# Kernel optimization log

Measured on AMD Instinct MI355X. Metric: run time of the kernel, lower is better.

Reference implementation:

```python
import jax, jax.numpy as jnp
import numpy as np

HEADS = 32
MAX_PERIOD = 10000.0
EPS = 1e-5


def layernorm(x, w, b):
    m = x.mean(-1, keepdims=True)
    v = ((x - m) ** 2).mean(-1, keepdims=True)
    return (x - m) * jax.lax.rsqrt(v + EPS) * w + b


def apply_rope(q, k, pos):
    # q, k: [B, T, H, D]; pos: [B, T] integer positions
    D = q.shape[-1]
    ds = D // 2
    inv_freq = 1.0 / (MAX_PERIOD ** (jnp.arange(ds, dtype=jnp.float32) / ds))
    ang = pos[..., None].astype(jnp.float32) * inv_freq          # [B, T, ds]
    cos = jnp.cos(ang)[:, :, None, :]                             # [B, T, 1, ds]
    sin = jnp.sin(ang)[:, :, None, :]

    def rot(t):
        tr, ti = t[..., 0::2], t[..., 1::2]
        out_r = tr * cos - ti * sin
        out_i = tr * sin + ti * cos
        return jnp.stack([out_r, out_i], axis=-1).reshape(t.shape)

    return rot(q), rot(k)


def setup_inputs() -> dict:
    key = jax.random.key(0)
    ks = jax.random.split(key, 8)
    B, T, C, F = 2, 1024, 2048, 8192
    H, D = HEADS, C // HEADS
    cap = 1024
    s = 0.02
    return {
        "x": jax.random.normal(ks[0], (B, T, C), jnp.float32),
        "cache": jnp.zeros((2, B, H, cap, D), jnp.float32),
        "in_proj_w": jax.random.normal(ks[1], (3 * C, C), jnp.float32) * s,
        "out_proj_w": jax.random.normal(ks[2], (C, C), jnp.float32) * s,
        "ln1_w": jnp.ones((C,), jnp.float32),
        "ln1_b": jnp.zeros((C,), jnp.float32),
        "ln2_w": jnp.ones((C,), jnp.float32),
        "ln2_b": jnp.zeros((C,), jnp.float32),
        "lin1_w": jax.random.normal(ks[3], (F, C), jnp.float32) * s,
        "lin2_w": jax.random.normal(ks[4], (C, F), jnp.float32) * s,
        "offset": jnp.zeros((B,), jnp.int64 if jax.config.jax_enable_x64 else jnp.int32),
        "end_offset": jnp.zeros((B,), jnp.int64 if jax.config.jax_enable_x64 else jnp.int32),
        "context": 512,
    }


def reference(x, cache, in_proj_w, out_proj_w, ln1_w, ln1_b, ln2_w, ln2_b,
              lin1_w, lin2_w, offset, end_offset, context):
    B, T, C = x.shape
    H = HEADS
    D = C // H
    cap = cache.shape[3]

    # ---- self-attention block ----
    h = layernorm(x, ln1_w, ln1_b)
    qkv = (h @ in_proj_w.T).reshape(B, T, 3, H, D)
    q, k, v = qkv[:, :, 0], qkv[:, :, 1], qkv[:, :, 2]           # [B, T, H, D]

    pos_q = offset[:, None] + jnp.arange(T)                       # [B, T]
    q, k = apply_rope(q, k, pos_q)

    q = q.transpose(0, 2, 1, 3)                                   # [B, H, T, D]
    k = k.transpose(0, 2, 1, 3)
    v = v.transpose(0, 2, 1, 3)

    # circular KV-cache update (functional version of `complete`)
    idx = (jnp.arange(T) + end_offset[:, None]) % cap             # [B, T]

    def upd(c, t, i):  # c: [H, cap, D], t: [H, T, D], i: [T]
        return c.at[:, i, :].set(t)

    keys = jax.vmap(upd)(cache[0], k, idx)                        # [B, H, cap, D]
    values = jax.vmap(upd)(cache[1], v, idx)

    slots = jnp.arange(cap)
    last = end_offset + T - 1                                     # [B]
    end_index = last % cap
    delta = slots[None, :] - end_index[:, None]                   # [B, cap]
    positions = jnp.where(delta <= 0, last[:, None] + delta,
                          last[:, None] + delta - cap)
    invalid = slots[None, :] >= (end_offset + T)[:, None]
    positions = jnp.where(invalid, -1, positions)                 # [B, cap]

    # sliding-window causal mask
    d = pos_q[:, :, None] - positions[:, None, :]                 # [B, T, cap]
    mask = (positions[:, None, :] >= 0) & (d >= 0) & (d < context)

    scale = 1.0 / jnp.sqrt(jnp.asarray(D, jnp.float32))
    scores = jnp.einsum('bhtd,bhsd->bhts', q, keys) * scale
    scores = jnp.where(mask[:, None], scores, jnp.asarray(-1e30, scores.dtype))
    attn = jax.nn.softmax(scores, axis=-1)
    o = jnp.einsum('bhts,bhsd->bhtd', attn, values)
    o = o.transpose(0, 2, 1, 3).reshape(B, T, C)
    x = x + o @ out_proj_w.T

    # ---- feed-forward block ----
    h2 = layernorm(x, ln2_w, ln2_b)
    ff = jax.nn.gelu(h2 @ lin1_w.T, approximate=False) @ lin2_w.T
    return x + ff
```

## Files before the change

kernel.cpp:

```cpp
#include <hip/hip_runtime.h>

typedef __attribute__((ext_vector_type(8))) short bf16x8;
typedef __attribute__((ext_vector_type(4))) float f32x4;
typedef __attribute__((ext_vector_type(8))) short short8v;
typedef __attribute__((ext_vector_type(4))) float float4v;

#define DEV static __device__ __forceinline__

DEV short f2bf(float f) {
  unsigned u = __builtin_bit_cast(unsigned, f);
  u = (u + 0x7fffu + ((u >> 16) & 1u)) >> 16;
  return (short)u;
}
DEV float bf2f(short s) {
  unsigned u = ((unsigned)(unsigned short)s) << 16;
  return __builtin_bit_cast(float, u);
}

DEV void gload_lds16(const void* g, void* l) {
  __builtin_amdgcn_global_load_lds((const __attribute__((address_space(1))) void*)g,
                                   (__attribute__((address_space(3))) void*)l, 16, 0, 0);
}

__global__ __launch_bounds__(256) void cvt_kernel(const float* __restrict__ src,
                                                  short* __restrict__ dst, int n8) {
  int i = blockIdx.x * 256 + threadIdx.x;
  const int stride = gridDim.x * 256;
  for (; i < n8; i += stride) {
    float4v a = ((const float4v*)src)[i * 2];
    float4v b = ((const float4v*)src)[i * 2 + 1];
    short8v o;
    o[0] = f2bf(a.x); o[1] = f2bf(a.y); o[2] = f2bf(a.z); o[3] = f2bf(a.w);
    o[4] = f2bf(b.x); o[5] = f2bf(b.y); o[6] = f2bf(b.z); o[7] = f2bf(b.w);
    ((short8v*)dst)[i] = o;
  }
}

__global__ __launch_bounds__(256) void ln_kernel(const float* __restrict__ x,
                                                 const float* __restrict__ w,
                                                 const float* __restrict__ b,
                                                 short* __restrict__ out) {
  const int C = 2048;
  const int row = blockIdx.x;
  const int tid = threadIdx.x;
  const float* xr = x + (size_t)row * C;
  float xv[8];
  *(float4v*)(xv) = *(const float4v*)(xr + tid * 8);
  *(float4v*)(xv + 4) = *(const float4v*)(xr + tid * 8 + 4);
  float s = 0.f, ss = 0.f;
#pragma unroll
  for (int i = 0; i < 8; ++i) { s += xv[i]; ss += xv[i] * xv[i]; }
#pragma unroll
  for (int d = 1; d < 64; d <<= 1) { s += __shfl_xor(s, d); ss += __shfl_xor(ss, d); }
  __shared__ float red[8];
  const int lane = tid & 63, wv = tid >> 6;
  if (lane == 0) { red[wv] = s; red[4 + wv] = ss; }
  __syncthreads();
  s = red[0] + red[1] + red[2] + red[3];
  ss = red[4] + red[5] + red[6] + red[7];
  const float mean = s * (1.f / 2048.f);
  const float var = ss * (1.f / 2048.f) - mean * mean;
  const float rs = rsqrtf(var + 1e-5f);
  float wv8[8], bv8[8];
  *(float4v*)(wv8) = *(const float4v*)(w + tid * 8);
  *(float4v*)(wv8 + 4) = *(const float4v*)(w + tid * 8 + 4);
  *(float4v*)(bv8) = *(const float4v*)(b + tid * 8);
  *(float4v*)(bv8 + 4) = *(const float4v*)(b + tid * 8 + 4);
  short8v o;
#pragma unroll
  for (int i = 0; i < 8; ++i) o[i] = f2bf((xv[i] - mean) * rs * wv8[i] + bv8[i]);
  *(short8v*)(out + (size_t)row * C + tid * 8) = o;
}

template <int EPI>
__global__ __launch_bounds__(512, 2) void gemm256(const short* __restrict__ A,
                                                  const short* __restrict__ Bw,
                                                  void* __restrict__ C0, void* __restrict__ C1,
                                                  void* __restrict__ C2, void* __restrict__ C3,
                                                  int N, int K, int kChunk, int kTiles) {
  extern __shared__ short smem[];
  const int tid = threadIdx.x;
  const int lane = tid & 63;
  const int wv = tid >> 6;
  const int wr = wv >> 2;
  const int wc = wv & 3;
  const int m0 = blockIdx.y * 256;
  const int n0 = blockIdx.x * 256;
  const int kBegin = blockIdx.z * kChunk;

  const int l15 = lane & 15;
  const int lg = lane >> 4;

  const int fa0 = tid, fa1 = tid + 512;
  const int rA0 = fa0 >> 2, rA1 = fa1 >> 2;
  const int cA0 = (((fa0 & 3) ^ ((rA0 >> 1) & 3))) * 8;
  const int cA1 = (((fa1 & 3) ^ ((rA1 >> 1) & 3))) * 8;

  const short* Asrc0 = A + (size_t)(m0 + rA0) * K + kBegin + cA0;
  const short* Asrc1 = A + (size_t)(m0 + rA1) * K + kBegin + cA1;
  const short* Bsrc0 = Bw + (size_t)(n0 + rA0) * K + kBegin + cA0;
  const short* Bsrc1 = Bw + (size_t)(n0 + rA1) * K + kBegin + cA1;

  f32x4 acc[8][4] = {};

#define STAGE(t)                                                        \
  {                                                                     \
    short* dstb = smem + (((t) & 3) * 16384);                           \
    const size_t ko = (size_t)(t) * 32;                                 \
    gload_lds16(Asrc0 + ko, dstb + fa0 * 8);                            \
    gload_lds16(Asrc1 + ko, dstb + fa1 * 8);                            \
    gload_lds16(Bsrc0 + ko, dstb + 8192 + fa0 * 8);                     \
    gload_lds16(Bsrc1 + ko, dstb + 8192 + fa1 * 8);                     \
  }

  const int pre = kTiles < 3 ? kTiles : 3;
  for (int p = 0; p < pre; ++p) STAGE(p);

  for (int t = 0; t < kTiles; ++t) {
    const int rem = kTiles - 1 - t;
    if (rem >= 2) {
      asm volatile("s_waitcnt vmcnt(8)" ::: "memory");
    } else if (rem == 1) {
      asm volatile("s_waitcnt vmcnt(4)" ::: "memory");
    } else {
      asm volatile("s_waitcnt vmcnt(0)" ::: "memory");
    }
    __builtin_amdgcn_sched_barrier(0);
    __builtin_amdgcn_s_barrier();
    __builtin_amdgcn_sched_barrier(0);

    if (t + 3 < kTiles) STAGE(t + 3);

    const short* sa = smem + ((t & 3) * 16384);
    const short* sb = sa + 8192;
    bf16x8 af[8], bf[4];
#pragma unroll
    for (int m = 0; m < 8; ++m) {
      const int row = wr * 128 + m * 16 + l15;
      af[m] = *(const bf16x8*)(sa + row * 32 + ((lg ^ ((row >> 1) & 3)) * 8));
    }
#pragma unroll
    for (int n = 0; n < 4; ++n) {
      const int row = wc * 64 + n * 16 + l15;
      bf[n] = *(const bf16x8*)(sb + row * 32 + ((lg ^ ((row >> 1) & 3)) * 8));
    }
    __builtin_amdgcn_s_setprio(1);
#pragma unroll
    for (int m = 0; m < 8; ++m)
#pragma unroll
      for (int n = 0; n < 4; ++n)
        acc[m][n] = __builtin_amdgcn_mfma_f32_16x16x32_bf16(af[m], bf[n], acc[m][n], 0, 0, 0);
    __builtin_amdgcn_s_setprio(0);
  }
#undef STAGE

  void* Cout = blockIdx.z == 0 ? C0 : blockIdx.z == 1 ? C1 : blockIdx.z == 2 ? C2 : C3;
#pragma unroll
  for (int m = 0; m < 8; ++m) {
#pragma unroll
    for (int n = 0; n < 4; ++n) {
#pragma unroll
      for (int r = 0; r < 4; ++r) {
        const size_t idx =
            (size_t)(m0 + wr * 128 + m * 16 + lg * 4 + r) * N + (n0 + wc * 64 + n * 16 + l15);
        const float v = acc[m][n][r];
        if (EPI == 0) {
          ((short*)Cout)[idx] = f2bf(v);
        } else if (EPI == 2) {
          const float gl = 0.5f * v * (1.f + erff(v * 0.70710678118f));
          ((short*)Cout)[idx] = f2bf(gl);
        } else {
          ((float*)Cout)[idx] = v;
        }
      }
    }
  }
}

__global__ __launch_bounds__(256) void reduce_k(float* __restrict__ dst,
                                                const float* __restrict__ resid,
                                                const float* __restrict__ p1,
                                                const float* __restrict__ p2,
                                                const float* __restrict__ p3,
                                                int ns, int n4) {
  int i = blockIdx.x * 256 + threadIdx.x;
  const int stride = gridDim.x * 256;
  for (; i < n4; i += stride) {
    float4v d = ((const float4v*)dst)[i];
    float4v r = ((const float4v*)resid)[i];
    float4v a = ((const float4v*)p1)[i];
    d.x += r.x + a.x; d.y += r.y + a.y; d.z += r.z + a.z; d.w += r.w + a.w;
    if (ns == 4) {
      float4v b = ((const float4v*)p2)[i];
      float4v c = ((const float4v*)p3)[i];
      d.x += b.x + c.x; d.y += b.y + c.y; d.z += b.z + c.z; d.w += b.w + c.w;
    }
    ((float4v*)dst)[i] = d;
  }
}

__global__ __launch_bounds__(256) void rope_kernel(const short* __restrict__ qkv,
                                                   short* __restrict__ qo,
                                                   short* __restrict__ ko,
                                                   short* __restrict__ vo,
                                                   const int* __restrict__ offset) {
  const int T = 1024, H = 32;
  const int g = blockIdx.x * 256 + threadIdx.x;
  const int j = g & 31;
  const int h = (g >> 5) & 31;
  const int t = (g >> 10) & 1023;
  const int b = g >> 20;
  const size_t inb = (size_t)(b * T + t) * 6144 + h * 64 + 2 * j;
  const size_t outb = (size_t)((b * H + h) * T + t) * 64 + 2 * j;
  const int pos = offset[b] + t;
  const float ang = (float)pos * __builtin_exp2f(-13.287712379549449f * (float)j * (1.f / 32.f));
  float sn, c;
  __sincosf(ang, &sn, &c);
  const float qr = bf2f(qkv[inb]), qi = bf2f(qkv[inb + 1]);
  qo[outb] = f2bf(qr * c - qi * sn);
  qo[outb + 1] = f2bf(qr * sn + qi * c);
  const float kr = bf2f(qkv[inb + 2048]), ki = bf2f(qkv[inb + 2048 + 1]);
  ko[outb] = f2bf(kr * c - ki * sn);
  ko[outb + 1] = f2bf(kr * sn + ki * c);
  vo[outb] = qkv[inb + 4096];
  vo[outb + 1] = qkv[inb + 4096 + 1];
}

__global__ __launch_bounds__(256) void attn_kernel(const short* __restrict__ qb,
                                                   const short* __restrict__ kb,
                                                   const short* __restrict__ vb,
                                                   short* __restrict__ o,
                                                   const int* __restrict__ offset,
                                                   const int* __restrict__ end_offset,
                                                   const int* __restrict__ ctxp) {
  const int T = 1024;
  __shared__ short Ks[64 * 64];
  __shared__ short Vt[64 * 64];
  __shared__ short Ps[4][16 * 64];
  const int tid = threadIdx.x;
  const int lane = tid & 63;
  const int w = tid >> 6;
  const int blk = blockIdx.x;
  const int qt = blk & 15;
  const int bh = blk >> 4;
  const int b = bh >> 5;
  const int h = bh & 31;
  const int q0 = qt * 64;
  const int offq = offset[b];
  const int offk = end_offset[b];
  const int W = ctxp[0];
  const int odelta = offq - offk;

  const short* qp = qb + (size_t)bh * T * 64;
  const short* kp = kb + (size_t)bh * T * 64;
  const short* vp = vb + (size_t)bh * T * 64;

  const int l15 = lane & 15;
  const int lg = lane >> 4;

  bf16x8 qf[2];
  {
    const int qrow = q0 + w * 16 + l15;
    qf[0] = *(const bf16x8*)(qp + (size_t)qrow * 64 + lg * 8);
    qf[1] = *(const bf16x8*)(qp + (size_t)qrow * 64 + 32 + lg * 8);
  }

  f32x4 oacc[4] = {};
  float mrow[4] = {-1e30f, -1e30f, -1e30f, -1e30f};
  float ssum[4] = {0.f, 0.f, 0.f, 0.f};

  int kv_lo = q0 + odelta - (W - 1);
  if (kv_lo < 0) kv_lo = 0;
  int kv_hi = q0 + 63 + odelta;
  if (kv_hi > T - 1) kv_hi = T - 1;

  for (int t0 = (kv_lo & ~63); t0 <= kv_hi; t0 += 64) {
    __syncthreads();
#pragma unroll
    for (int j = 0; j < 2; ++j) {
      const int r0 = (j * 4 + w) * 8;
      gload_lds16(kp + (size_t)(t0 + r0 + (lane >> 3)) * 64 + (lane & 7) * 8, Ks + r0 * 64);
    }
#pragma unroll
    for (int j = 0; j < 2; ++j) {
      const int kv = (tid >> 3) + j * 32;
      const int d0 = (tid & 7) * 8;
      bf16x8 vv = *(const bf16x8*)(vp + (size_t)(t0 + kv) * 64 + d0);
#pragma unroll
      for (int i = 0; i < 8; ++i) Vt[(d0 + i) * 64 + kv] = vv[i];
    }
    __syncthreads();

    f32x4 s[4] = {};
#pragma unroll
    for (int n = 0; n < 4; ++n) {
      bf16x8 k0f = *(const bf16x8*)(Ks + (n * 16 + l15) * 64 + lg * 8);
      bf16x8 k1f = *(const bf16x8*)(Ks + (n * 16 + l15) * 64 + 32 + lg * 8);
      s[n] = __builtin_amdgcn_mfma_f32_16x16x32_bf16(qf[0], k0f, s[n], 0, 0, 0);
      s[n] = __builtin_amdgcn_mfma_f32_16x16x32_bf16(qf[1], k1f, s[n], 0, 0, 0);
    }

#pragma unroll
    for (int r = 0; r < 4; ++r) {
      const int tq = q0 + w * 16 + lg * 4 + r;
      float sv[4];
      float mx = -1e30f;
#pragma unroll
      for (int n = 0; n < 4; ++n) {
        const int tk = t0 + n * 16 + l15;
        const int dd = tq + odelta - tk;
        const bool valid = (dd >= 0) && (dd < W);
        sv[n] = valid ? s[n][r] * 0.125f : -1e30f;
        mx = fmaxf(mx, sv[n]);
      }
      mx = fmaxf(mx, __shfl_xor(mx, 1));
      mx = fmaxf(mx, __shfl_xor(mx, 2));
      mx = fmaxf(mx, __shfl_xor(mx, 4));
      mx = fmaxf(mx, __shfl_xor(mx, 8));
      const float mnew = fmaxf(mrow[r], mx);
      const float sf = __expf(mrow[r] - mnew);
      mrow[r] = mnew;
      float ls = 0.f;
#pragma unroll
      for (int n = 0; n < 4; ++n) {
        const float p = (sv[n] > -0.5e30f) ? __expf(sv[n] - mnew) : 0.f;
        ls += p;
        Ps[w][(lg * 4 + r) * 64 + n * 16 + l15] = f2bf(p);
      }
      ls += __shfl_xor(ls, 1);
      ls += __shfl_xor(ls, 2);
      ls += __shfl_xor(ls, 4);
      ls += __shfl_xor(ls, 8);
      ssum[r] = ssum[r] * sf + ls;
#pragma unroll
      for (int n = 0; n < 4; ++n) oacc[n][r] *= sf;
    }

#pragma unroll
    for (int ks = 0; ks < 2; ++ks) {
      bf16x8 pa = *(const bf16x8*)(&Ps[w][l15 * 64 + ks * 32 + lg * 8]);
#pragma unroll
      for (int n = 0; n < 4; ++n) {
        bf16x8 vf = *(const bf16x8*)(Vt + (n * 16 + l15) * 64 + ks * 32 + lg * 8);
        oacc[n] = __builtin_amdgcn_mfma_f32_16x16x32_bf16(pa, vf, oacc[n], 0, 0, 0);
      }
    }
  }

#pragma unroll
  for (int n = 0; n < 4; ++n) {
#pragma unroll
    for (int r = 0; r < 4; ++r) {
      const int tq = q0 + w * 16 + lg * 4 + r;
      const float val = oacc[n][r] / ssum[r];
      o[(size_t)(b * T + tq) * 2048 + h * 64 + n * 16 + l15] = f2bf(val);
    }
  }
}

extern "C" void kernel_launch(void* const* d_in, const int* in_sizes, int n_in,
                              void* d_out, int out_size, void* d_ws, size_t ws_size,
                              hipStream_t stream) {
  (void)in_sizes; (void)n_in; (void)out_size;
  const float* x          = (const float*)d_in[0];
  const float* in_proj_w  = (const float*)d_in[2];
  const float* out_proj_w = (const float*)d_in[3];
  const float* ln1_w      = (const float*)d_in[4];
  const float* ln1_b      = (const float*)d_in[5];
  const float* ln2_w      = (const float*)d_in[6];
  const float* ln2_b      = (const float*)d_in[7];
  const float* lin1_w     = (const float*)d_in[8];
  const float* lin2_w     = (const float*)d_in[9];
  const int* offset       = (const int*)d_in[10];
  const int* end_offset   = (const int*)d_in[11];
  const int* ctx          = (const int*)d_in[12];
  float* out = (float*)d_out;

  hipFuncSetAttribute((const void*)gemm256<0>, hipFuncAttributeMaxDynamicSharedMemorySize, 131072);
  hipFuncSetAttribute((const void*)gemm256<2>, hipFuncAttributeMaxDynamicSharedMemorySize, 131072);
  hipFuncSetAttribute((const void*)gemm256<3>, hipFuncAttributeMaxDynamicSharedMemorySize, 131072);

  const size_t MiB = 1048576;
  char* ws = (char*)d_ws;
  float* x1    = (float*)(ws);
  short* hbuf  = (short*)(ws + 16 * MiB);
  short* qkv   = (short*)(ws + 24 * MiB);
  short* qr    = (short*)(ws + 48 * MiB);
  short* kr    = (short*)(ws + 56 * MiB);
  short* vr    = (short*)(ws + 64 * MiB);
  short* wb_in = (short*)(ws + 48 * MiB);
  short* wb_out= (short*)(ws + 24 * MiB);
  float* p1o   = (float*)(ws + 32 * MiB);
  short* g     = (short*)(ws + 24 * MiB);
  short* wb1   = (short*)(ws + 64 * MiB);
  short* wb2   = (short*)(ws + 56 * MiB);
  float* p1f   = (float*)(ws + 72 * MiB);
  float* p2f   = (float*)(ws + 88 * MiB);
  float* p3f   = (float*)(ws + 104 * MiB);
  const int NS_FF2 = (ws_size >= 121 * MiB) ? 4 : 2;

  ln_kernel<<<2048, 256, 0, stream>>>(x, ln1_w, ln1_b, hbuf);
  cvt_kernel<<<2048, 256, 0, stream>>>(in_proj_w, wb_in, 12582912 / 8);
  gemm256<0><<<dim3(24, 8, 1), 512, 131072, stream>>>(hbuf, wb_in, qkv, nullptr, nullptr, nullptr,
                                                      6144, 2048, 2048, 64);
  rope_kernel<<<8192, 256, 0, stream>>>(qkv, qr, kr, vr, offset);
  attn_kernel<<<1024, 256, 0, stream>>>(qr, kr, vr, hbuf, offset, end_offset, ctx);
  cvt_kernel<<<2048, 256, 0, stream>>>(out_proj_w, wb_out, 4194304 / 8);
  gemm256<3><<<dim3(8, 8, 2), 512, 131072, stream>>>(hbuf, wb_out, x1, p1o, nullptr, nullptr,
                                                     2048, 2048, 1024, 32);
  reduce_k<<<1024, 256, 0, stream>>>(x1, x, p1o, nullptr, nullptr, 2, 1048576);
  ln_kernel<<<2048, 256, 0, stream>>>(x1, ln2_w, ln2_b, hbuf);
  cvt_kernel<<<2048, 256, 0, stream>>>(lin1_w, wb1, 16777216 / 8);
  gemm256<2><<<dim3(32, 8, 1), 512, 131072, stream>>>(hbuf, wb1, g, nullptr, nullptr, nullptr,
                                                      8192, 2048, 2048, 64);
  cvt_kernel<<<2048, 256, 0, stream>>>(lin2_w, wb2, 16777216 / 8);
  if (NS_FF2 == 4) {
    gemm256<3><<<dim3(8, 8, 4), 512, 131072, stream>>>(g, wb2, out, p1f, p2f, p3f,
                                                       2048, 8192, 2048, 64);
    reduce_k<<<1024, 256, 0, stream>>>(out, x1, p1f, p2f, p3f, 4, 1048576);
  } else {
    gemm256<3><<<dim3(8, 8, 2), 512, 131072, stream>>>(g, wb2, out, p1f, nullptr, nullptr,
                                                       2048, 8192, 4096, 128);
    reduce_k<<<1024, 256, 0, stream>>>(out, x1, p1f, nullptr, nullptr, 2, 1048576);
  }
}
```

Before: 432.6 us.

## Remap GEMM tiles per XCD, deepen out-proj split-K, bf16 FF2 partials

Block indices in the GEMM are remapped so each group of 8 consecutive blocks (one per XCD) covers a compact rectangle of output tiles. The aim is better L2 reuse of A and B tiles within each XCD's cache. The out-projection split-K goes from 2 to 4 slices to raise parallelism. The FF2 GEMM is fixed at 2-way split-K with the second partial stored as bf16 and merged by a new reduction kernel, which cuts partial-sum traffic at some precision cost.

```diff
diff --git a/kernel.cpp b/kernel.cpp
--- a/kernel.cpp
+++ b/kernel.cpp
@@ -53,8 +53,8 @@
 #pragma unroll
   for (int d = 1; d < 64; d <<= 1) { s += __shfl_xor(s, d); ss += __shfl_xor(ss, d); }
   __shared__ float red[8];
-  const int lane = tid & 63, wv = tid >> 6;
-  if (lane == 0) { red[wv] = s; red[4 + wv] = ss; }
+  const int lane = tid & 63, wvv = tid >> 6;
+  if (lane == 0) { red[wvv] = s; red[4 + wvv] = ss; }
   __syncthreads();
   s = red[0] + red[1] + red[2] + red[3];
   ss = red[4] + red[5] + red[6] + red[7];
@@ -77,15 +77,19 @@
                                                   const short* __restrict__ Bw,
                                                   void* __restrict__ C0, void* __restrict__ C1,
                                                   void* __restrict__ C2, void* __restrict__ C3,
-                                                  int N, int K, int kChunk, int kTiles) {
+                                                  int N, int K, int kChunk, int kTiles,
+                                                  int rtx, int rty, int nrx) {
   extern __shared__ short smem[];
   const int tid = threadIdx.x;
   const int lane = tid & 63;
   const int wv = tid >> 6;
   const int wr = wv >> 2;
   const int wc = wv & 3;
-  const int m0 = blockIdx.y * 256;
-  const int n0 = blockIdx.x * 256;
+  const int f2 = blockIdx.y * gridDim.x + blockIdx.x;
+  const int xcd = f2 & 7, q = f2 >> 3;
+  const int rx = xcd % nrx, ry = xcd / nrx;
+  const int m0 = (ry * rty + q / rtx) * 256;
+  const int n0 = (rx * rtx + q % rtx) * 256;
   const int kBegin = blockIdx.z * kChunk;
 
   const int l15 = lane & 15;
@@ -169,8 +173,13 @@
         } else if (EPI == 2) {
           const float gl = 0.5f * v * (1.f + erff(v * 0.70710678118f));
           ((short*)Cout)[idx] = f2bf(gl);
+        } else if (EPI == 3) {
+          ((float*)Cout)[idx] = v;
         } else {
-          ((float*)Cout)[idx] = v;
+          if (blockIdx.z == 0)
+            ((float*)Cout)[idx] = v;
+          else
+            ((short*)Cout)[idx] = f2bf(v);
         }
       }
     }
@@ -196,6 +205,27 @@
       d.x += b.x + c.x; d.y += b.y + c.y; d.z += b.z + c.z; d.w += b.w + c.w;
     }
     ((float4v*)dst)[i] = d;
+  }
+}
+
+__global__ __launch_bounds__(256) void reduce_kb(float* __restrict__ dst,
+                                                 const float* __restrict__ resid,
+                                                 const short* __restrict__ p1,
+                                                 int n8) {
+  int i = blockIdx.x * 256 + threadIdx.x;
+  const int stride = gridDim.x * 256;
+  for (; i < n8; i += stride) {
+    float4v d0 = ((const float4v*)dst)[i * 2];
+    float4v d1 = ((const float4v*)dst)[i * 2 + 1];
+    float4v r0 = ((const float4v*)resid)[i * 2];
+    float4v r1 = ((const float4v*)resid)[i * 2 + 1];
+    short8v p = ((const short8v*)p1)[i];
+    d0.x += r0.x + bf2f(p[0]); d0.y += r0.y + bf2f(p[1]);
+    d0.z += r0.z + bf2f(p[2]); d0.w += r0.w + bf2f(p[3]);
+    d1.x += r1.x + bf2f(p[4]); d1.y += r1.y + bf2f(p[5]);
+    d1.z += r1.z + bf2f(p[6]); d1.w += r1.w + bf2f(p[7]);
+    ((float4v*)dst)[i * 2] = d0;
+    ((float4v*)dst)[i * 2 + 1] = d1;
   }
 }
 
@@ -361,7 +391,7 @@
 extern "C" void kernel_launch(void* const* d_in, const int* in_sizes, int n_in,
                               void* d_out, int out_size, void* d_ws, size_t ws_size,
                               hipStream_t stream) {
-  (void)in_sizes; (void)n_in; (void)out_size;
+  (void)in_sizes; (void)n_in; (void)out_size; (void)ws_size;
   const float* x          = (const float*)d_in[0];
   const float* in_proj_w  = (const float*)d_in[2];
   const float* out_proj_w = (const float*)d_in[3];
@@ -379,6 +409,7 @@
   hipFuncSetAttribute((const void*)gemm256<0>, hipFuncAttributeMaxDynamicSharedMemorySize, 131072);
   hipFuncSetAttribute((const void*)gemm256<2>, hipFuncAttributeMaxDynamicSharedMemorySize, 131072);
   hipFuncSetAttribute((const void*)gemm256<3>, hipFuncAttributeMaxDynamicSharedMemorySize, 131072);
+  hipFuncSetAttribute((const void*)gemm256<4>, hipFuncAttributeMaxDynamicSharedMemorySize, 131072);
 
   const size_t MiB = 1048576;
   char* ws = (char*)d_ws;
@@ -391,36 +422,29 @@
   short* wb_in = (short*)(ws + 48 * MiB);
   short* wb_out= (short*)(ws + 24 * MiB);
   float* p1o   = (float*)(ws + 32 * MiB);
+  float* p2o   = (float*)(ws + 48 * MiB);
+  float* p3o   = (float*)(ws + 64 * MiB);
   short* g     = (short*)(ws + 24 * MiB);
   short* wb1   = (short*)(ws + 64 * MiB);
   short* wb2   = (short*)(ws + 56 * MiB);
-  float* p1f   = (float*)(ws + 72 * MiB);
-  float* p2f   = (float*)(ws + 88 * MiB);
-  float* p3f   = (float*)(ws + 104 * MiB);
-  const int NS_FF2 = (ws_size >= 121 * MiB) ? 4 : 2;
+  short* p1b   = (short*)(ws + 16 * MiB);
 
   ln_kernel<<<2048, 256, 0, stream>>>(x, ln1_w, ln1_b, hbuf);
   cvt_kernel<<<2048, 256, 0, stream>>>(in_proj_w, wb_in, 12582912 / 8);
   gemm256<0><<<dim3(24, 8, 1), 512, 131072, stream>>>(hbuf, wb_in, qkv, nullptr, nullptr, nullptr,
-                                                      6144, 2048, 2048, 64);
+                                                      6144, 2048, 2048, 64, 6, 4, 4);
   rope_kernel<<<8192, 256, 0, stream>>>(qkv, qr, kr, vr, offset);
   attn_kernel<<<1024, 256, 0, stream>>>(qr, kr, vr, hbuf, offset, end_offset, ctx);
   cvt_kernel<<<2048, 256, 0, stream>>>(out_proj_w, wb_out, 4194304 / 8);
-  gemm256<3><<<dim3(8, 8, 2), 512, 131072, stream>>>(hbuf, wb_out, x1, p1o, nullptr, nullptr,
-                                                     2048, 2048, 1024, 32);
-  reduce_k<<<1024, 256, 0, stream>>>(x1, x, p1o, nullptr, nullptr, 2, 1048576);
+  gemm256<3><<<dim3(8, 8, 4), 512, 131072, stream>>>(hbuf, wb_out, x1, p1o, p2o, p3o,
+                                                     2048, 2048, 512, 16, 4, 2, 2);
+  reduce_k<<<1024, 256, 0, stream>>>(x1, x, p1o, p2o, p3o, 4, 1048576);
   ln_kernel<<<2048, 256, 0, stream>>>(x1, ln2_w, ln2_b, hbuf);
   cvt_kernel<<<2048, 256, 0, stream>>>(lin1_w, wb1, 16777216 / 8);
   gemm256<2><<<dim3(32, 8, 1), 512, 131072, stream>>>(hbuf, wb1, g, nullptr, nullptr, nullptr,
-                                                      8192, 2048, 2048, 64);
+                                                      8192, 2048, 2048, 64, 8, 4, 4);
   cvt_kernel<<<2048, 256, 0, stream>>>(lin2_w, wb2, 16777216 / 8);
-  if (NS_FF2 == 4) {
-    gemm256<3><<<dim3(8, 8, 4), 512, 131072, stream>>>(g, wb2, out, p1f, p2f, p3f,
-                                                       2048, 8192, 2048, 64);
-    reduce_k<<<1024, 256, 0, stream>>>(out, x1, p1f, p2f, p3f, 4, 1048576);
-  } else {
-    gemm256<3><<<dim3(8, 8, 2), 512, 131072, stream>>>(g, wb2, out, p1f, nullptr, nullptr,
-                                                       2048, 8192, 4096, 128);
-    reduce_k<<<1024, 256, 0, stream>>>(out, x1, p1f, nullptr, nullptr, 2, 1048576);
-  }
-}
+  gemm256<4><<<dim3(8, 8, 2), 512, 131072, stream>>>(g, wb2, out, p1b, nullptr, nullptr,
+                                                     2048, 8192, 4096, 128, 4, 2, 2);
+  reduce_kb<<<1024, 256, 0, stream>>>(out, x1, p1b, 524288);
+}
```

Result: slower. 493.0 us (+14.0%).
